# Performance work log

Measured on AMD Instinct MI355X. Metric: run time of the kernel, lower is better.

The kernel has to match this reference:

```python
import jax, jax.numpy as jnp
import numpy as np

B, S, H = 1, 2048, 2048
NH, NKV, HD = 16, 4, 128
N_REP = NH // NKV
WINDOW = 1024
THETA = 10000.0


def _rope(x, fc):
    # x: [B,S,h,HD]; fc: [B,S,HD//2,2] (cos,sin)
    xr = x.reshape(*x.shape[:-1], HD // 2, 2)
    a, b = xr[..., 0], xr[..., 1]
    cos = fc[:, :, None, :, 0]
    sin = fc[:, :, None, :, 1]
    out = jnp.stack((a * cos - b * sin, a * sin + b * cos), axis=-1)
    return out.reshape(x.shape)


def setup_inputs() -> dict:
    key = jax.random.key(0)
    ks = jax.random.split(key, 5)
    hidden_state = jax.random.normal(ks[0], (B, S, H), jnp.float32)
    # rotary table: cos/sin of pos * theta^{-2i/d}
    inv_freq = 1.0 / (THETA ** (jnp.arange(0, HD, 2, dtype=jnp.float32) / HD))
    ang = jnp.arange(S, dtype=jnp.float32)[:, None] * inv_freq[None, :]  # [S, HD//2]
    freq_cis = jnp.stack((jnp.cos(ang), jnp.sin(ang)), axis=-1)  # [S, HD//2, 2]
    attention_mask = jnp.ones((B, S), dtype=bool)
    i = jnp.arange(S)[:, None]
    j = jnp.arange(S)[None, :]
    causal_mask = ((j <= i) & (i - j < WINDOW))[None, None]  # [1,1,S,S] sliding-window causal
    position_ids = jnp.broadcast_to(jnp.arange(S, dtype=jnp.int32), (B, S))
    scale = 0.02
    Wq = jax.random.normal(ks[1], (H, NH * HD), jnp.float32) * scale
    Wk = jax.random.normal(ks[2], (H, NKV * HD), jnp.float32) * scale
    Wv = jax.random.normal(ks[3], (H, NKV * HD), jnp.float32) * scale
    Wo = jax.random.normal(ks[4], (NH * HD, H), jnp.float32) * scale
    return {"hidden_state": hidden_state, "freq_cis": freq_cis,
            "attention_mask": attention_mask, "causal_mask": causal_mask,
            "position_ids": position_ids, "Wq": Wq, "Wk": Wk, "Wv": Wv, "Wo": Wo}


def reference(hidden_state, freq_cis, attention_mask, causal_mask, position_ids,
              Wq, Wk, Wv, Wo):
    q = (hidden_state @ Wq).reshape(B, S, NH, HD)
    k = (hidden_state @ Wk).reshape(B, S, NKV, HD)
    v = (hidden_state @ Wv).reshape(B, S, NKV, HD)
    fc = freq_cis[position_ids]  # [B,S,HD//2,2]
    q = _rope(q, fc)
    k = _rope(k, fc)
    # GQA: repeat kv heads (contiguous groups, as in repeat_kv)
    k = jnp.repeat(k, N_REP, axis=2)  # [B,S,NH,HD]
    v = jnp.repeat(v, N_REP, axis=2)
    mask = causal_mask & attention_mask[:, None, None, :]  # [B,1,S,S]
    bias = jnp.where(mask, 0.0, jnp.finfo(jnp.float32).min)
    scores = jnp.einsum('bqhd,bkhd->bhqk', q, k) * (1.0 / np.sqrt(HD))
    attn = jax.nn.softmax(scores + bias, axis=-1)
    out = jnp.einsum('bhqk,bkhd->bqhd', attn, v).reshape(B, S, NH * HD)
    return out @ Wo
```

## Files before the change

kernel.cpp:

```cpp
#include <hip/hip_runtime.h>
#include <hip/hip_bf16.h>
#include <stdint.h>

#define S_LEN 2048
#define HDIM  2048
#define NHQ   16
#define NKVH  4
#define HD    128
#define WIN   1024
#define SM_SCALE 0.08838834764831845f
#define NEG_BIG  -1.0e30f

typedef __attribute__((ext_vector_type(8))) short short8;
typedef __attribute__((ext_vector_type(4))) float float4v;
typedef unsigned short u16;

static __device__ __forceinline__ float bf2f(u16 u) {
  union { unsigned int i; float f; } v; v.i = ((unsigned int)u) << 16; return v.f;
}
static __device__ __forceinline__ u16 f2bf(float f) {
  union { float f; unsigned int i; } v; v.f = f;
  unsigned int x = v.i;
  return (u16)((x + 0x7fffu + ((x >> 16) & 1u)) >> 16);
}

__global__ __launch_bounds__(256) void prep(
    const float* __restrict__ hs, const float* __restrict__ Wq,
    const float* __restrict__ Wk, const float* __restrict__ Wv,
    const float* __restrict__ Wo, u16* __restrict__ hsB,
    u16* __restrict__ WqkvT, u16* __restrict__ WoT)
{
  const int b = blockIdx.x;
  if (b < 1024) {
    u16* dst = hsB + (size_t)b * 4096;
    const int mb = b >> 6, ks = b & 63;
#pragma unroll
    for (int i = 0; i < 2; ++i) {
      const int cid = i * 256 + threadIdx.x;
      const int kc  = cid & 3;
      const int m   = cid >> 2;
      const float* src = hs + ((size_t)(mb * 128 + m)) * 2048 + ks * 32 + kc * 8;
      const float4 v0 = *(const float4*)src;
      const float4 v1 = *(const float4*)(src + 4);
      short8 o;
      o[0] = (short)f2bf(v0.x); o[1] = (short)f2bf(v0.y);
      o[2] = (short)f2bf(v0.z); o[3] = (short)f2bf(v0.w);
      o[4] = (short)f2bf(v1.x); o[5] = (short)f2bf(v1.y);
      o[6] = (short)f2bf(v1.z); o[7] = (short)f2bf(v1.w);
      *(short8*)(dst + (kc * 128 + m) * 8) = o;
    }
    return;
  }

  __shared__ u16 t[32][33];
  const int tx = threadIdx.x & 31, ty = threadIdx.x >> 5;
  int n0, kstep;
  const float* W; u16* DT; int nsrc, N;
  if (b < 7168) {
    const int bb = b - 1024;
    n0    = (bb % 96) * 32;
    kstep = bb / 96;
    if (n0 < 2048)      { W = Wq; nsrc = n0;        N = 2048; }
    else if (n0 < 2560) { W = Wk; nsrc = n0 - 2048; N = 512;  }
    else                { W = Wv; nsrc = n0 - 2560; N = 512;  }
    DT = WqkvT;
  } else {
    const int bb = b - 7168;
    n0    = (bb & 63) * 32;
    kstep = bb >> 6;
    W = Wo; nsrc = n0; N = 2048; DT = WoT;
  }
  const int k0 = kstep * 32;

#pragma unroll
  for (int i = 0; i < 4; ++i)
    t[ty + i * 8][tx] = f2bf(W[(size_t)(k0 + ty + i * 8) * N + nsrc + tx]);
  __syncthreads();
  const int kc = tx >> 3, e = tx & 7;
#pragma unroll
  for (int i = 0; i < 4; ++i) {
    const int n = n0 + ty + i * 8;
    DT[((size_t)((n >> 6) * 64 + kstep)) * 2048 + kc * 512 + (n & 63) * 8 + e]
        = t[tx][ty + i * 8];
  }
}

template <int EPI>
__global__ __launch_bounds__(256) void gemm_bt(
    const u16* __restrict__ Apk, const u16* __restrict__ Bpk,
    void* __restrict__ Cv, const float* __restrict__ fc,
    u16* __restrict__ Qb, u16* __restrict__ Kp, u16* __restrict__ Vp,
    int M, int N, int K)
{
  __shared__ u16 Als[4096];
  __shared__ u16 Bls[2048];

  const int tid  = threadIdx.x;
  const int lane = tid & 63;
  const int w    = tid >> 6;
  const int quad = lane >> 4;
  const int lc   = lane & 15;
  const int n0   = blockIdx.x * 64;
  const int m0   = blockIdx.y * 128;
  const int wr   = (w >> 1) * 64;
  const int wc   = (w & 1) * 32;
  const int ktiles = K >> 5;

  float4v acc[4][2];
#pragma unroll
  for (int i = 0; i < 4; ++i)
#pragma unroll
    for (int j = 0; j < 2; ++j) acc[i][j] = (float4v){0.f, 0.f, 0.f, 0.f};

  for (int ks = 0; ks < ktiles; ++ks) {
    const char* ab = (const char*)(Apk + ((size_t)((m0 >> 7) * ktiles + ks)) * 4096);
    const char* bb = (const char*)(Bpk + ((size_t)((n0 >> 6) * ktiles + ks)) * 2048);
    __syncthreads();
#pragma unroll
    for (int r = 0; r < 2; ++r) {
      const int off = r * 4096 + tid * 16;
      __builtin_amdgcn_global_load_lds(
          (__attribute__((address_space(1))) void*)(ab + off),
          (__attribute__((address_space(3))) void*)((char*)Als + off), 16, 0, 0);
    }
    {
      const int off = tid * 16;
      __builtin_amdgcn_global_load_lds(
          (__attribute__((address_space(1))) void*)(bb + off),
          (__attribute__((address_space(3))) void*)((char*)Bls + off), 16, 0, 0);
    }
    __syncthreads();

    short8 af[4], bfr[2];
#pragma unroll
    for (int mi = 0; mi < 4; ++mi)
      af[mi] = *(const short8*)(Als + quad * 1024 + (wr + mi * 16 + lc) * 8);
#pragma unroll
    for (int ni = 0; ni < 2; ++ni)
      bfr[ni] = *(const short8*)(Bls + quad * 512 + (wc + ni * 16 + lc) * 8);
#pragma unroll
    for (int mi = 0; mi < 4; ++mi)
#pragma unroll
      for (int ni = 0; ni < 2; ++ni)
        acc[mi][ni] = __builtin_amdgcn_mfma_f32_16x16x32_bf16(
            af[mi], bfr[ni], acc[mi][ni], 0, 0, 0);
  }

  if (EPI == 0) {
#pragma unroll
    for (int mi = 0; mi < 4; ++mi)
#pragma unroll
      for (int ni = 0; ni < 2; ++ni)
#pragma unroll
        for (int r = 0; r < 4; ++r) {
          const int row = m0 + wr + mi * 16 + quad * 4 + r;
          const int col = n0 + wc + ni * 16 + lc;
          ((float*)Cv)[(size_t)row * N + col] = acc[mi][ni][r];
        }
  } else {
    if (n0 < 2560) {
#pragma unroll
      for (int mi = 0; mi < 4; ++mi)
#pragma unroll
        for (int ni = 0; ni < 2; ++ni)
#pragma unroll
          for (int r = 0; r < 4; ++r) {
            const int row = m0 + wr + mi * 16 + quad * 4 + r;
            const int col = n0 + wc + ni * 16 + lc;
            const int hh  = col & 127;
            const float v = acc[mi][ni][r];
            const float p = __shfl_xor(v, 1);
            const float2 cs = *(const float2*)(fc + row * 128 + (hh & ~1));
            const float res = (col & 1) ? (p * cs.y + v * cs.x)
                                        : (v * cs.x - p * cs.y);
            if (n0 < 2048) {
              Qb[(size_t)row * 2048 + col] = f2bf(res);
            } else {
              const int kvh = (col - 2048) >> 7;
              const int kt  = row >> 6, key = row & 63;
              const int c   = hh >> 3, e = hh & 7;
              Kp[((size_t)(kvh * 32 + kt)) * 8192 + key * 128
                 + ((c ^ (key & 15)) * 8) + e] = f2bf(res);
            }
          }
    } else {
#pragma unroll
      for (int mi = 0; mi < 4; ++mi)
#pragma unroll
        for (int ni = 0; ni < 2; ++ni)
#pragma unroll
          for (int r = 0; r < 4; ++r) {
            const int row = m0 + wr + mi * 16 + quad * 4 + r;
            const int col = n0 + wc + ni * 16 + lc;
            const int kvh = (col - 2560) >> 7;
            const int hd  = col & 127;
            const int kt  = row >> 6, key = row & 63;
            const int c   = (key >> 3) ^ (hd & 7);
            Vp[((size_t)(kvh * 32 + kt)) * 8192 + hd * 64 + c * 8 + (key & 7)]
                = f2bf(acc[mi][ni][r]);
          }
    }
  }
}

__global__ __launch_bounds__(256) void attn_kernel(
    const u16* __restrict__ Qb, const u16* __restrict__ kp,
    const u16* __restrict__ vp, u16* __restrict__ out)
{
  __shared__ u16 Kls[64 * 128];
  __shared__ u16 Vls[128 * 64];
  __shared__ u16 P[4 * 16 * 72];

  const int tid  = threadIdx.x;
  const int lane = tid & 63;
  const int w    = tid >> 6;
  const int quad = lane >> 4;
  const int lc   = lane & 15;
  const int q0   = blockIdx.x * 64;
  const int h    = blockIdx.y;
  const int kvh  = h >> 2;
  const int rb   = q0 + w * 16;

  short8 qf[4];
  {
    const u16* qp = Qb + (size_t)(rb + lc) * 2048 + h * HD + quad * 8;
#pragma unroll
    for (int ks = 0; ks < 4; ++ks) qf[ks] = *(const short8*)(qp + ks * 32);
  }

  float4v o[8];
#pragma unroll
  for (int i = 0; i < 8; ++i) o[i] = (float4v){0.f, 0.f, 0.f, 0.f};
  float mrow[4], lrow[4];
#pragma unroll
  for (int r = 0; r < 4; ++r) { mrow[r] = NEG_BIG; lrow[r] = 0.f; }

  int jmin_blk = q0 - (WIN - 1); if (jmin_blk < 0) jmin_blk = 0;
  const int kt_begin = jmin_blk >> 6;
  const int kt_end   = q0 >> 6;

  const size_t tbase = (size_t)(kvh * 32) * 8192;

  for (int kt = kt_begin; kt <= kt_end; ++kt) {
    const int k0 = kt * 64;

    __syncthreads();
    {
      const u16* kg = kp + tbase + (size_t)kt * 8192;
      const u16* vg = vp + tbase + (size_t)kt * 8192;
#pragma unroll
      for (int i = 0; i < 4; ++i) {
        const int off = i * 4096 + tid * 16;
        __builtin_amdgcn_global_load_lds(
            (__attribute__((address_space(1))) void*)((const char*)kg + off),
            (__attribute__((address_space(3))) void*)((char*)Kls + off), 16, 0, 0);
        __builtin_amdgcn_global_load_lds(
            (__attribute__((address_space(1))) void*)((const char*)vg + off),
            (__attribute__((address_space(3))) void*)((char*)Vls + off), 16, 0, 0);
      }
    }
    __syncthreads();

    if (k0 > rb + 15 || k0 + 63 < rb - (WIN - 1)) continue;

    float4v sacc[4];
#pragma unroll
    for (int i = 0; i < 4; ++i) sacc[i] = (float4v){0.f, 0.f, 0.f, 0.f};
#pragma unroll
    for (int ks = 0; ks < 4; ++ks) {
#pragma unroll
      for (int nt = 0; nt < 4; ++nt) {
        const int key = nt * 16 + lc;
        const int c   = (ks * 4 + quad) ^ (key & 15);
        short8 kb = *(const short8*)(Kls + key * 128 + c * 8);
        sacc[nt] = __builtin_amdgcn_mfma_f32_16x16x32_bf16(qf[ks], kb, sacc[nt], 0, 0, 0);
      }
    }

    const bool full = (k0 + 63 <= rb) && ((rb + 15 - k0) <= WIN - 1);
    float sv[4][4];
    bool  ok[4][4];
    float rmax[4] = {NEG_BIG, NEG_BIG, NEG_BIG, NEG_BIG};
#pragma unroll
    for (int nt = 0; nt < 4; ++nt) {
      const int j = k0 + nt * 16 + lc;
#pragma unroll
      for (int r = 0; r < 4; ++r) {
        const int i = rb + quad * 4 + r;
        const bool valid = full || ((j <= i) && (i - j < WIN));
        float s = sacc[nt][r] * SM_SCALE;
        s = valid ? s : NEG_BIG;
        sv[nt][r] = s;
        ok[nt][r] = valid;
        rmax[r] = fmaxf(rmax[r], s);
      }
    }
#pragma unroll
    for (int off = 1; off < 16; off <<= 1)
#pragma unroll
      for (int r = 0; r < 4; ++r)
        rmax[r] = fmaxf(rmax[r], __shfl_xor(rmax[r], off, 64));

    float alpha[4], rsum[4];
#pragma unroll
    for (int r = 0; r < 4; ++r) {
      const float mn = fmaxf(mrow[r], rmax[r]);
      alpha[r] = __expf(mrow[r] - mn);
      mrow[r] = mn;
      rsum[r] = 0.f;
    }
#pragma unroll
    for (int nt = 0; nt < 4; ++nt)
#pragma unroll
      for (int r = 0; r < 4; ++r) {
        const float p = ok[nt][r] ? __expf(sv[nt][r] - mrow[r]) : 0.f;
        rsum[r] += p;
        P[(w * 16 + quad * 4 + r) * 72 + nt * 16 + lc] = f2bf(p);
      }
#pragma unroll
    for (int off = 1; off < 16; off <<= 1)
#pragma unroll
      for (int r = 0; r < 4; ++r)
        rsum[r] += __shfl_xor(rsum[r], off, 64);
#pragma unroll
    for (int r = 0; r < 4; ++r) lrow[r] = lrow[r] * alpha[r] + rsum[r];
#pragma unroll
    for (int i = 0; i < 8; ++i)
#pragma unroll
      for (int r = 0; r < 4; ++r) o[i][r] *= alpha[r];

#pragma unroll
    for (int ktk = 0; ktk < 2; ++ktk) {
      short8 pa = *(const short8*)(P + (w * 16 + lc) * 72 + ktk * 32 + quad * 8);
#pragma unroll
      for (int nt2 = 0; nt2 < 8; ++nt2) {
        const int hd = nt2 * 16 + lc;
        const int c  = (ktk * 4 + quad) ^ (hd & 7);
        short8 vb = *(const short8*)(Vls + hd * 64 + c * 8);
        o[nt2] = __builtin_amdgcn_mfma_f32_16x16x32_bf16(pa, vb, o[nt2], 0, 0, 0);
      }
    }
  }

#pragma unroll
  for (int r = 0; r < 4; ++r) {
    const float inv = (lrow[r] > 0.f) ? (1.f / lrow[r]) : 0.f;
    const int row = rb + quad * 4 + r;
    const size_t mbase = (size_t)(row >> 7) * 64;
    const int m = row & 127;
#pragma unroll
    for (int nt2 = 0; nt2 < 8; ++nt2) {
      const int col = h * HD + nt2 * 16 + lc;
      const int kstep = col >> 5, kc = (col >> 3) & 3, e = col & 7;
      out[(mbase + kstep) * 4096 + kc * 1024 + m * 8 + e] = f2bf(o[nt2][r] * inv);
    }
  }
}

extern "C" void kernel_launch(void* const* d_in, const int* in_sizes, int n_in,
                              void* d_out, int out_size, void* d_ws, size_t ws_size,
                              hipStream_t stream) {
  const float* hs = (const float*)d_in[0];
  const float* fc = (const float*)d_in[1];
  const float* Wq = (const float*)d_in[5];
  const float* Wk = (const float*)d_in[6];
  const float* Wv = (const float*)d_in[7];
  const float* Wo = (const float*)d_in[8];
  float* outp = (float*)d_out;

  u16* hsB   = (u16*)d_ws;
  u16* WqkvT = hsB   + (size_t)2048 * 2048;
  u16* WoT   = WqkvT + (size_t)3072 * 2048;
  u16* Qb    = WoT   + (size_t)2048 * 2048;
  u16* ATTN  = Qb    + (size_t)2048 * 2048;
  u16* Kp    = ATTN  + (size_t)2048 * 2048;
  u16* Vp    = Kp    + (size_t)4 * 2048 * 128;

  dim3 blk(256);
  prep<<<dim3(11264), blk, 0, stream>>>(hs, Wq, Wk, Wv, Wo, hsB, WqkvT, WoT);
  gemm_bt<1><<<dim3(3072 / 64, 2048 / 128), blk, 0, stream>>>(
      hsB, WqkvT, nullptr, fc, Qb, Kp, Vp, 2048, 3072, 2048);
  attn_kernel<<<dim3(2048 / 64, NHQ), blk, 0, stream>>>(Qb, Kp, Vp, ATTN);
  gemm_bt<0><<<dim3(2048 / 64, 2048 / 128), blk, 0, stream>>>(
      ATTN, WoT, outp, nullptr, nullptr, nullptr, nullptr, 2048, 2048, 2048);
}
```

Before: 263.9 us.

## Double-buffer GEMM and attention LDS tiles, reorder attention blocks, skip rescale

Both the projection GEMM and the attention kernel now double-buffer their LDS tiles, so the next K-tile (or K/V tile) loads while the current one is consumed, and only one barrier remains per iteration. The GEMM also stages two k-steps per buffer. The attention grid is flattened to 1D with a mirrored query-tile order, intended to balance heavy and light sliding-window tiles across dispatch. The online-softmax rescale now runs only when some row max grows, and s_setprio is raised around the MFMA sections. These add extra LDS (48KB for the GEMM, 68KB-plus for attention), which may lower occupancy.

```diff
diff --git a/kernel.cpp b/kernel.cpp
--- a/kernel.cpp
+++ b/kernel.cpp
@@ -92,8 +92,8 @@
     u16* __restrict__ Qb, u16* __restrict__ Kp, u16* __restrict__ Vp,
     int M, int N, int K)
 {
-  __shared__ u16 Als[4096];
-  __shared__ u16 Bls[2048];
+  __shared__ u16 Als[2][8192];
+  __shared__ u16 Bls[2][4096];
 
   const int tid  = threadIdx.x;
   const int lane = tid & 63;
@@ -105,6 +105,10 @@
   const int wr   = (w >> 1) * 64;
   const int wc   = (w & 1) * 32;
   const int ktiles = K >> 5;
+  const int nk2    = ktiles >> 1;
+
+  const char* aB = (const char*)(Apk + (size_t)(m0 >> 7) * ktiles * 4096);
+  const char* bB = (const char*)(Bpk + (size_t)(n0 >> 6) * ktiles * 2048);
 
   float4v acc[4][2];
 #pragma unroll
@@ -112,38 +116,50 @@
 #pragma unroll
     for (int j = 0; j < 2; ++j) acc[i][j] = (float4v){0.f, 0.f, 0.f, 0.f};
 
-  for (int ks = 0; ks < ktiles; ++ks) {
-    const char* ab = (const char*)(Apk + ((size_t)((m0 >> 7) * ktiles + ks)) * 4096);
-    const char* bb = (const char*)(Bpk + ((size_t)((n0 >> 6) * ktiles + ks)) * 2048);
-    __syncthreads();
+  auto stage = [&](int bi, int kk) {
+    const char* ab = aB + (size_t)kk * 16384;
+    const char* bb = bB + (size_t)kk * 8192;
+#pragma unroll
+    for (int r = 0; r < 4; ++r) {
+      const int off = r * 4096 + tid * 16;
+      __builtin_amdgcn_global_load_lds(
+          (__attribute__((address_space(1))) void*)(ab + off),
+          (__attribute__((address_space(3))) void*)((char*)Als[bi] + off), 16, 0, 0);
+    }
 #pragma unroll
     for (int r = 0; r < 2; ++r) {
       const int off = r * 4096 + tid * 16;
       __builtin_amdgcn_global_load_lds(
-          (__attribute__((address_space(1))) void*)(ab + off),
-          (__attribute__((address_space(3))) void*)((char*)Als + off), 16, 0, 0);
-    }
-    {
-      const int off = tid * 16;
-      __builtin_amdgcn_global_load_lds(
           (__attribute__((address_space(1))) void*)(bb + off),
-          (__attribute__((address_space(3))) void*)((char*)Bls + off), 16, 0, 0);
+          (__attribute__((address_space(3))) void*)((char*)Bls[bi] + off), 16, 0, 0);
+    }
+  };
+
+  stage(0, 0);
+  __syncthreads();
+  int cur = 0;
+  for (int kk = 0; kk < nk2; ++kk) {
+    if (kk + 1 < nk2) stage(cur ^ 1, kk + 1);
+#pragma unroll
+    for (int half = 0; half < 2; ++half) {
+      const u16* Ab = Als[cur] + half * 4096;
+      const u16* Bb = Bls[cur] + half * 2048;
+      short8 af[4], bfr[2];
+#pragma unroll
+      for (int mi = 0; mi < 4; ++mi)
+        af[mi] = *(const short8*)(Ab + quad * 1024 + (wr + mi * 16 + lc) * 8);
+#pragma unroll
+      for (int ni = 0; ni < 2; ++ni)
+        bfr[ni] = *(const short8*)(Bb + quad * 512 + (wc + ni * 16 + lc) * 8);
+#pragma unroll
+      for (int mi = 0; mi < 4; ++mi)
+#pragma unroll
+        for (int ni = 0; ni < 2; ++ni)
+          acc[mi][ni] = __builtin_amdgcn_mfma_f32_16x16x32_bf16(
+              af[mi], bfr[ni], acc[mi][ni], 0, 0, 0);
     }
     __syncthreads();
-
-    short8 af[4], bfr[2];
-#pragma unroll
-    for (int mi = 0; mi < 4; ++mi)
-      af[mi] = *(const short8*)(Als + quad * 1024 + (wr + mi * 16 + lc) * 8);
-#pragma unroll
-    for (int ni = 0; ni < 2; ++ni)
-      bfr[ni] = *(const short8*)(Bls + quad * 512 + (wc + ni * 16 + lc) * 8);
-#pragma unroll
-    for (int mi = 0; mi < 4; ++mi)
-#pragma unroll
-      for (int ni = 0; ni < 2; ++ni)
-        acc[mi][ni] = __builtin_amdgcn_mfma_f32_16x16x32_bf16(
-            af[mi], bfr[ni], acc[mi][ni], 0, 0, 0);
+    cur ^= 1;
   }
 
   if (EPI == 0) {
@@ -207,8 +223,8 @@
     const u16* __restrict__ Qb, const u16* __restrict__ kp,
     const u16* __restrict__ vp, u16* __restrict__ out)
 {
-  __shared__ u16 Kls[64 * 128];
-  __shared__ u16 Vls[128 * 64];
+  __shared__ u16 Kls[2][64 * 128];
+  __shared__ u16 Vls[2][128 * 64];
   __shared__ u16 P[4 * 16 * 72];
 
   const int tid  = threadIdx.x;
@@ -216,8 +232,13 @@
   const int w    = tid >> 6;
   const int quad = lane >> 4;
   const int lc   = lane & 15;
-  const int q0   = blockIdx.x * 64;
-  const int h    = blockIdx.y;
+
+  const int b    = blockIdx.x;
+  const int ii   = b & 255;
+  const int tt   = ii >> 4;
+  const int t    = (b >> 8) ? (31 - tt) : tt;
+  const int q0   = t * 64;
+  const int h    = ii & 15;
   const int kvh  = h >> 2;
   const int rb   = q0 + w * 16;
 
@@ -241,105 +262,119 @@
 
   const size_t tbase = (size_t)(kvh * 32) * 8192;
 
+  auto stageKV = [&](int bi, int ktt) {
+    const char* kg = (const char*)(kp + tbase + (size_t)ktt * 8192);
+    const char* vg = (const char*)(vp + tbase + (size_t)ktt * 8192);
+#pragma unroll
+    for (int i = 0; i < 4; ++i) {
+      const int off = i * 4096 + tid * 16;
+      __builtin_amdgcn_global_load_lds(
+          (__attribute__((address_space(1))) void*)(kg + off),
+          (__attribute__((address_space(3))) void*)((char*)Kls[bi] + off), 16, 0, 0);
+      __builtin_amdgcn_global_load_lds(
+          (__attribute__((address_space(1))) void*)(vg + off),
+          (__attribute__((address_space(3))) void*)((char*)Vls[bi] + off), 16, 0, 0);
+    }
+  };
+
+  stageKV(0, kt_begin);
+  __syncthreads();
+  int cur = 0;
+
   for (int kt = kt_begin; kt <= kt_end; ++kt) {
+    if (kt < kt_end) stageKV(cur ^ 1, kt + 1);
     const int k0 = kt * 64;
 
+    if (!(k0 > rb + 15 || k0 + 63 < rb - (WIN - 1))) {
+      float4v sacc[4];
+#pragma unroll
+      for (int i = 0; i < 4; ++i) sacc[i] = (float4v){0.f, 0.f, 0.f, 0.f};
+      __builtin_amdgcn_s_setprio(1);
+#pragma unroll
+      for (int ks = 0; ks < 4; ++ks) {
+#pragma unroll
+        for (int nt = 0; nt < 4; ++nt) {
+          const int key = nt * 16 + lc;
+          const int c   = (ks * 4 + quad) ^ (key & 15);
+          short8 kb = *(const short8*)(Kls[cur] + key * 128 + c * 8);
+          sacc[nt] = __builtin_amdgcn_mfma_f32_16x16x32_bf16(qf[ks], kb, sacc[nt], 0, 0, 0);
+        }
+      }
+      __builtin_amdgcn_s_setprio(0);
+
+      const bool full = (k0 + 63 <= rb) && ((rb + 15 - k0) <= WIN - 1);
+      float sv[4][4];
+      bool  ok[4][4];
+      float rmax[4] = {NEG_BIG, NEG_BIG, NEG_BIG, NEG_BIG};
+#pragma unroll
+      for (int nt = 0; nt < 4; ++nt) {
+        const int j = k0 + nt * 16 + lc;
+#pragma unroll
+        for (int r = 0; r < 4; ++r) {
+          const int i = rb + quad * 4 + r;
+          const bool valid = full || ((j <= i) && (i - j < WIN));
+          float s = sacc[nt][r] * SM_SCALE;
+          s = valid ? s : NEG_BIG;
+          sv[nt][r] = s;
+          ok[nt][r] = valid;
+          rmax[r] = fmaxf(rmax[r], s);
+        }
+      }
+#pragma unroll
+      for (int off = 1; off < 16; off <<= 1)
+#pragma unroll
+        for (int r = 0; r < 4; ++r)
+          rmax[r] = fmaxf(rmax[r], __shfl_xor(rmax[r], off, 64));
+
+      bool grow = false;
+#pragma unroll
+      for (int r = 0; r < 4; ++r) grow |= (rmax[r] > mrow[r]);
+      if (__any((int)grow)) {
+#pragma unroll
+        for (int r = 0; r < 4; ++r) {
+          const float mn = fmaxf(mrow[r], rmax[r]);
+          const float a  = __expf(mrow[r] - mn);
+          mrow[r] = mn;
+          lrow[r] *= a;
+#pragma unroll
+          for (int i = 0; i < 8; ++i) o[i][r] *= a;
+        }
+      }
+
+      float rsum[4] = {0.f, 0.f, 0.f, 0.f};
+#pragma unroll
+      for (int nt = 0; nt < 4; ++nt)
+#pragma unroll
+        for (int r = 0; r < 4; ++r) {
+          const float p = ok[nt][r] ? __expf(sv[nt][r] - mrow[r]) : 0.f;
+          rsum[r] += p;
+          P[(w * 16 + quad * 4 + r) * 72 + nt * 16 + lc] = f2bf(p);
+        }
+#pragma unroll
+      for (int off = 1; off < 16; off <<= 1)
+#pragma unroll
+        for (int r = 0; r < 4; ++r)
+          rsum[r] += __shfl_xor(rsum[r], off, 64);
+#pragma unroll
+      for (int r = 0; r < 4; ++r) lrow[r] += rsum[r];
+
+      __builtin_amdgcn_s_setprio(1);
+#pragma unroll
+      for (int ktk = 0; ktk < 2; ++ktk) {
+        short8 pa = *(const short8*)(P + (w * 16 + lc) * 72 + ktk * 32 + quad * 8);
+#pragma unroll
+        for (int nt2 = 0; nt2 < 8; ++nt2) {
+          const int hd = nt2 * 16 + lc;
+          const int c  = (ktk * 4 + quad) ^ (hd & 7);
+          short8 vb = *(const short8*)(Vls[cur] + hd * 64 + c * 8);
+          o[nt2] = __builtin_amdgcn_mfma_f32_16x16x32_bf16(pa, vb, o[nt2], 0, 0, 0);
+        }
+      }
+      __builtin_amdgcn_s_setprio(0);
+    }
+
     __syncthreads();
-    {
-      const u16* kg = kp + tbase + (size_t)kt * 8192;
-      const u16* vg = vp + tbase + (size_t)kt * 8192;
-#pragma unroll
-      for (int i = 0; i < 4; ++i) {
-        const int off = i * 4096 + tid * 16;
-        __builtin_amdgcn_global_load_lds(
-            (__attribute__((address_space(1))) void*)((const char*)kg + off),
-            (__attribute__((address_space(3))) void*)((char*)Kls + off), 16, 0, 0);
-        __builtin_amdgcn_global_load_lds(
-            (__attribute__((address_space(1))) void*)((const char*)vg + off),
-            (__attribute__((address_space(3))) void*)((char*)Vls + off), 16, 0, 0);
-      }
-    }
-    __syncthreads();
-
-    if (k0 > rb + 15 || k0 + 63 < rb - (WIN - 1)) continue;
-
-    float4v sacc[4];
-#pragma unroll
-    for (int i = 0; i < 4; ++i) sacc[i] = (float4v){0.f, 0.f, 0.f, 0.f};
-#pragma unroll
-    for (int ks = 0; ks < 4; ++ks) {
-#pragma unroll
-      for (int nt = 0; nt < 4; ++nt) {
-        const int key = nt * 16 + lc;
-        const int c   = (ks * 4 + quad) ^ (key & 15);
-        short8 kb = *(const short8*)(Kls + key * 128 + c * 8);
-        sacc[nt] = __builtin_amdgcn_mfma_f32_16x16x32_bf16(qf[ks], kb, sacc[nt], 0, 0, 0);
-      }
-    }
-
-    const bool full = (k0 + 63 <= rb) && ((rb + 15 - k0) <= WIN - 1);
-    float sv[4][4];
-    bool  ok[4][4];
-    float rmax[4] = {NEG_BIG, NEG_BIG, NEG_BIG, NEG_BIG};
-#pragma unroll
-    for (int nt = 0; nt < 4; ++nt) {
-      const int j = k0 + nt * 16 + lc;
-#pragma unroll
-      for (int r = 0; r < 4; ++r) {
-        const int i = rb + quad * 4 + r;
-        const bool valid = full || ((j <= i) && (i - j < WIN));
-        float s = sacc[nt][r] * SM_SCALE;
-        s = valid ? s : NEG_BIG;
-        sv[nt][r] = s;
-        ok[nt][r] = valid;
-        rmax[r] = fmaxf(rmax[r], s);
-      }
-    }
-#pragma unroll
-    for (int off = 1; off < 16; off <<= 1)
-#pragma unroll
-      for (int r = 0; r < 4; ++r)
-        rmax[r] = fmaxf(rmax[r], __shfl_xor(rmax[r], off, 64));
-
-    float alpha[4], rsum[4];
-#pragma unroll
-    for (int r = 0; r < 4; ++r) {
-      const float mn = fmaxf(mrow[r], rmax[r]);
-      alpha[r] = __expf(mrow[r] - mn);
-      mrow[r] = mn;
-      rsum[r] = 0.f;
-    }
-#pragma unroll
-    for (int nt = 0; nt < 4; ++nt)
-#pragma unroll
-      for (int r = 0; r < 4; ++r) {
-        const float p = ok[nt][r] ? __expf(sv[nt][r] - mrow[r]) : 0.f;
-        rsum[r] += p;
-        P[(w * 16 + quad * 4 + r) * 72 + nt * 16 + lc] = f2bf(p);
-      }
-#pragma unroll
-    for (int off = 1; off < 16; off <<= 1)
-#pragma unroll
-      for (int r = 0; r < 4; ++r)
-        rsum[r] += __shfl_xor(rsum[r], off, 64);
-#pragma unroll
-    for (int r = 0; r < 4; ++r) lrow[r] = lrow[r] * alpha[r] + rsum[r];
-#pragma unroll
-    for (int i = 0; i < 8; ++i)
-#pragma unroll
-      for (int r = 0; r < 4; ++r) o[i][r] *= alpha[r];
-
-#pragma unroll
-    for (int ktk = 0; ktk < 2; ++ktk) {
-      short8 pa = *(const short8*)(P + (w * 16 + lc) * 72 + ktk * 32 + quad * 8);
-#pragma unroll
-      for (int nt2 = 0; nt2 < 8; ++nt2) {
-        const int hd = nt2 * 16 + lc;
-        const int c  = (ktk * 4 + quad) ^ (hd & 7);
-        short8 vb = *(const short8*)(Vls + hd * 64 + c * 8);
-        o[nt2] = __builtin_amdgcn_mfma_f32_16x16x32_bf16(pa, vb, o[nt2], 0, 0, 0);
-      }
-    }
+    cur ^= 1;
   }
 
 #pragma unroll
@@ -380,7 +415,7 @@
   prep<<<dim3(11264), blk, 0, stream>>>(hs, Wq, Wk, Wv, Wo, hsB, WqkvT, WoT);
   gemm_bt<1><<<dim3(3072 / 64, 2048 / 128), blk, 0, stream>>>(
       hsB, WqkvT, nullptr, fc, Qb, Kp, Vp, 2048, 3072, 2048);
-  attn_kernel<<<dim3(2048 / 64, NHQ), blk, 0, stream>>>(Qb, Kp, Vp, ATTN);
+  attn_kernel<<<dim3(512), blk, 0, stream>>>(Qb, Kp, Vp, ATTN);
   gemm_bt<0><<<dim3(2048 / 64, 2048 / 128), blk, 0, stream>>>(
       ATTN, WoT, outp, nullptr, nullptr, nullptr, nullptr, 2048, 2048, 2048);
 }
```

Result: faster. 236.4 us (-10.4%).
